# Kernel optimization log

Measured on AMD Instinct MI355X. Metric: run time of the kernel, lower is better.

The kernel has to match this reference:

```python
import jax, jax.numpy as jnp
import numpy as np

N = 50000
E = 1_600_000
IN_C = 128
HID = 64
HEADS = 2
OUT_C = 16
NEG_SLOPE = 0.2
EPS = 1e-16


def setup_inputs() -> dict:
    key = jax.random.key(0)
    ks = jax.random.split(key, 10)
    x = jax.random.normal(ks[0], (N, IN_C), dtype=jnp.float32)
    edge_index = jax.random.randint(ks[1], (2, E), 0, N, dtype=jnp.int64)
    # layer 1: in -> HEADS * HID, concat=True
    s1 = 1.0 / np.sqrt(IN_C)
    W1 = jax.random.normal(ks[2], (IN_C, HEADS * HID), dtype=jnp.float32) * s1
    att_src1 = jax.random.normal(ks[3], (HEADS, HID), dtype=jnp.float32) * (1.0 / np.sqrt(HID))
    att_dst1 = jax.random.normal(ks[4], (HEADS, HID), dtype=jnp.float32) * (1.0 / np.sqrt(HID))
    b1 = jnp.zeros((HEADS * HID,), dtype=jnp.float32)
    # layer 2: HEADS*HID -> OUT_C, heads=1
    s2 = 1.0 / np.sqrt(HEADS * HID)
    W2 = jax.random.normal(ks[5], (HEADS * HID, OUT_C), dtype=jnp.float32) * s2
    att_src2 = jax.random.normal(ks[6], (1, OUT_C), dtype=jnp.float32) * (1.0 / np.sqrt(OUT_C))
    att_dst2 = jax.random.normal(ks[7], (1, OUT_C), dtype=jnp.float32) * (1.0 / np.sqrt(OUT_C))
    b2 = jnp.zeros((OUT_C,), dtype=jnp.float32)
    return {"x": x, "W1": W1, "att_src1": att_src1, "att_dst1": att_dst1, "b1": b1,
            "W2": W2, "att_src2": att_src2, "att_dst2": att_dst2, "b2": b2,
            "edge_index": edge_index}


def gat_conv(x, edge_index, W, att_src, att_dst, bias, heads, out_ch):
    """PyG-style GATConv: per-head linear, additive attention, softmax over
    incoming edges of each destination node, scatter-add aggregation."""
    n = x.shape[0]
    src, dst = edge_index[0], edge_index[1]
    h = (x @ W).reshape(n, heads, out_ch)                # [N,H,C]
    a_src = jnp.einsum('nhc,hc->nh', h, att_src)          # [N,H]
    a_dst = jnp.einsum('nhc,hc->nh', h, att_dst)          # [N,H]
    e = a_src[src] + a_dst[dst]                           # [E,H]
    e = jnp.where(e >= 0, e, NEG_SLOPE * e)               # LeakyReLU(0.2)
    e_max = jax.ops.segment_max(e, dst, num_segments=n)   # [N,H]
    e_max = jax.lax.stop_gradient(jnp.where(jnp.isfinite(e_max), e_max, 0.0))
    e_exp = jnp.exp(e - e_max[dst])                       # [E,H]
    denom = jax.ops.segment_sum(e_exp, dst, num_segments=n)  # [N,H]
    alpha = e_exp / (denom[dst] + EPS)                    # [E,H]
    msg = h[src] * alpha[:, :, None]                      # [E,H,C] (dominant traffic)
    out = jax.ops.segment_sum(msg, dst, num_segments=n)   # [N,H,C]
    return out.reshape(n, heads * out_ch) + bias


def reference(x, W1, att_src1, att_dst1, b1, W2, att_src2, att_dst2, b2, edge_index):
    h = gat_conv(x, edge_index, W1, att_src1, att_dst1, b1, HEADS, HID)
    h = jax.nn.elu(h)
    h = gat_conv(h, edge_index, W2, att_src2, att_dst2, b2, 1, OUT_C)
    return jax.nn.softmax(h, axis=1)
```

## Files before the change

### kernel.cpp

```cpp
#include <hip/hip_runtime.h>
#include <hip/hip_fp16.h>
#include <cstdint>
#include <cstddef>

#define N_NODES 50000
#define N_EDGES 1600000
#define NEG_SLOPE 0.2f
#define GAT_EPS 1e-16f

#define NCHUNK 128
#define CE (N_EDGES / NCHUNK)
#define NBKT 196
#define GEMM_BLOCKS 782

typedef _Float16 half8v __attribute__((ext_vector_type(8)));
typedef _Float16 half4v __attribute__((ext_vector_type(4)));
typedef float f32x4 __attribute__((ext_vector_type(4)));



__global__ __launch_bounds__(256) void k_gh(
    const float* __restrict__ x, const float* __restrict__ W1,
    const float* __restrict__ W2, const float* __restrict__ b1,
    const float* __restrict__ att_src, const float* __restrict__ att_dst,
    _Float16* __restrict__ h1p, float* __restrict__ a_src, float* __restrict__ a_dst,
    const int* __restrict__ ei, int* __restrict__ coarse,
    float* __restrict__ w2tp, float* __restrict__ b1p) {
    __shared__ __align__(16) char smem[34816];
    int t = threadIdx.x;
    int b = blockIdx.x;
    if (b == GEMM_BLOCKS + NCHUNK) {
        for (int i = t; i < 2112; i += 256) {
            int j = i / 132, kp = i % 132;
            float v = 0.f;
            if (kp < 128) {
                int real = (kp & 7) * 16 + (kp >> 3);
                v = W2[real * 16 + j];
            }
            w2tp[i] = v;
        }
        if (t < 128) {
            int real = (t & 7) * 16 + (t >> 3);
            b1p[t] = b1[real];
        }
        return;
    }
    if (b >= GEMM_BLOCKS) {
        int* h = (int*)smem;
        int g = b - GEMM_BLOCKS;
        int wv = t >> 6;
        for (int i = t; i < 1024; i += 256) h[i] = 0;
        __syncthreads();
        int* hw = h + (wv << 8);
        int e0 = g * CE;
        for (int e = e0 + t; e < e0 + CE; e += 256)
            atomicAdd(&hw[ei[N_EDGES + e] >> 8], 1);
        __syncthreads();
        if (t < NBKT) coarse[t * NCHUNK + g] = h[t] + h[256 + t] + h[512 + t] + h[768 + t];
        return;
    }
    _Float16* wl = (_Float16*)smem;
    for (int j = t; j < 16384; j += 256) {
        int k = j >> 7, c = j & 127;
        wl[c * 136 + k] = (_Float16)W1[j];
    }
    __syncthreads();
    int wv = t >> 6, lane = t & 63;
    int m = lane & 15, q = lane >> 4;
    int nb = b * 64 + wv * 16;
    int grow = nb + m;
    const float* xrow = x + (size_t)((grow < N_NODES) ? grow : (N_NODES - 1)) * 128;
    f32x4 acc[8];
#pragma unroll
    for (int ct = 0; ct < 8; ++ct) acc[ct] = (f32x4){0.f, 0.f, 0.f, 0.f};
#pragma unroll
    for (int kc = 0; kc < 4; ++kc) {
        float4 u0 = *(const float4*)(xrow + kc * 32 + q * 8);
        float4 u1 = *(const float4*)(xrow + kc * 32 + q * 8 + 4);
        half8v a;
        a[0] = (_Float16)u0.x; a[1] = (_Float16)u0.y;
        a[2] = (_Float16)u0.z; a[3] = (_Float16)u0.w;
        a[4] = (_Float16)u1.x; a[5] = (_Float16)u1.y;
        a[6] = (_Float16)u1.z; a[7] = (_Float16)u1.w;
#pragma unroll
        for (int ct = 0; ct < 8; ++ct) {
            half8v bf = *(const half8v*)(wl + (ct * 16 + m) * 136 + kc * 32 + q * 8);
            acc[ct] = __builtin_amdgcn_mfma_f32_16x16x32_f16(a, bf, acc[ct], 0, 0, 0);
        }
    }
    float att_s[8], att_d[8];
#pragma unroll
    for (int ct = 0; ct < 8; ++ct) {
        att_s[ct] = att_src[ct * 16 + m];
        att_d[ct] = att_dst[ct * 16 + m];
    }
#pragma unroll
    for (int r = 0; r < 4; ++r) {
        int gn = nb + q * 4 + r;
        half8v hv;
        float ps0 = 0.f, ps1 = 0.f, pd0 = 0.f, pd1 = 0.f;
#pragma unroll
        for (int ct = 0; ct < 8; ++ct) {
            float v = acc[ct][r];
            hv[ct] = (_Float16)v;
            if (ct < 4) { ps0 += v * att_s[ct]; pd0 += v * att_d[ct]; }
            else        { ps1 += v * att_s[ct]; pd1 += v * att_d[ct]; }
        }
#pragma unroll
        for (int off = 8; off >= 1; off >>= 1) {
            ps0 += __shfl_xor(ps0, off, 64);
            ps1 += __shfl_xor(ps1, off, 64);
            pd0 += __shfl_xor(pd0, off, 64);
            pd1 += __shfl_xor(pd1, off, 64);
        }
        if (gn < N_NODES) {
            *(half8v*)(h1p + (size_t)gn * 128 + m * 8) = hv;
            if (m == 0) {
                a_src[gn * 2 + 0] = ps0;
                a_src[gn * 2 + 1] = ps1;
                a_dst[gn * 2 + 0] = pd0;
                a_dst[gn * 2 + 1] = pd1;
            }
        }
    }
}


__global__ __launch_bounds__(1024) void k_cscan(const int* __restrict__ coarse,
                                                int* __restrict__ cbase,
                                                int* __restrict__ bb,
                                                int* __restrict__ row_start) {
    __shared__ int cl[NBKT * NCHUNK];
    __shared__ int btot[256];
    __shared__ int bbase[NBKT];
    __shared__ int wt4[4];
    int t = threadIdx.x;
    for (int i = t; i < NBKT * NCHUNK; i += 1024) cl[i] = coarse[i];
    __syncthreads();
    if (t < 256) {
        int s = 0;
        if (t < NBKT)
            for (int g = 0; g < NCHUNK; ++g) s += cl[t * NCHUNK + g];
        btot[t] = s;
        int lane = t & 63, w = t >> 6;
        int x = s;
#pragma unroll
        for (int off = 1; off < 64; off <<= 1) {
            int y = __shfl_up(x, off, 64);
            if (lane >= off) x += y;
        }
        if (lane == 63) wt4[w] = x;
        __syncthreads();
        int woff = 0;
        for (int i = 0; i < w; ++i) woff += wt4[i];
        if (t < NBKT) bbase[t] = woff + x - s;
    } else {
        __syncthreads();
    }
    __syncthreads();
    if (t < NBKT) {
        int run = bbase[t];
        bb[t] = run;
        for (int g = 0; g < NCHUNK; ++g) {
            cbase[t * NCHUNK + g] = run;
            run += cl[t * NCHUNK + g];
        }
    }
    if (t == 0) { bb[NBKT] = N_EDGES; row_start[N_NODES] = N_EDGES; }
}

__global__ __launch_bounds__(256) void k_partition(const int* __restrict__ ei,
                                                   const int* __restrict__ cbase,
                                                   unsigned int* __restrict__ part) {
    __shared__ int loc[NBKT];
    int t = threadIdx.x, g = blockIdx.x;
    if (t < NBKT) loc[t] = cbase[t * NCHUNK + g];
    __syncthreads();
    int e0 = g * CE;
    for (int e = e0 + t; e < e0 + CE; e += 256) {
        int s = ei[e], d = ei[N_EDGES + e];
        int slot = atomicAdd(&loc[d >> 8], 1);
        part[slot] = ((unsigned int)d << 16) | (unsigned int)s;
    }
}

__global__ __launch_bounds__(256) void k_local(const unsigned int* __restrict__ part,
                                               const int* __restrict__ bb,
                                               const float* __restrict__ a_src1,
                                               const float* __restrict__ a_dst1,
                                               int* __restrict__ row_start,
                                               int* __restrict__ csrc,
                                               float2* __restrict__ cw) {
    __shared__ int hist[256];
    __shared__ int fillv[256];
    __shared__ float2 adl[256];
    __shared__ int wtot[4];
    int t = threadIdx.x, b = blockIdx.x;
    int n0 = b << 8;
    int es = bb[b], ee = bb[b + 1];
    hist[t] = 0;
    if (n0 + t < N_NODES) adl[t] = ((const float2*)a_dst1)[n0 + t];
    __syncthreads();
    for (int e = es + t; e < ee; e += 256) atomicAdd(&hist[(part[e] >> 16) - n0], 1);
    __syncthreads();
    int lane = t & 63, w = t >> 6;
    int v = hist[t], x = v;
#pragma unroll
    for (int off = 1; off < 64; off <<= 1) {
        int y = __shfl_up(x, off, 64);
        if (lane >= off) x += y;
    }
    if (lane == 63) wtot[w] = x;
    __syncthreads();
    int woff = 0;
    for (int i = 0; i < w; ++i) woff += wtot[i];
    int excl = woff + x - v;
    if (n0 + t < N_NODES) row_start[n0 + t] = es + excl;
    fillv[t] = excl;
    __syncthreads();
    for (int e = es + t; e < ee; e += 256) {
        unsigned int sd = part[e];
        int s = (int)(sd & 0xFFFFu);
        int j = (int)(sd >> 16) - n0;
        int slot = es + atomicAdd(&fillv[j], 1);
        float2 as = ((const float2*)a_src1)[s];
        float2 ad = adl[j];
        float e0 = as.x + ad.x; e0 = (e0 >= 0.f) ? e0 : NEG_SLOPE * e0;
        float e1 = as.y + ad.y; e1 = (e1 >= 0.f) ? e1 : NEG_SLOPE * e1;
        csrc[slot] = s;
        cw[slot] = make_float2(expf(e0), expf(e1));
    }
}


__global__ __launch_bounds__(256) void k_agg1f(
    const int* __restrict__ row_start, const int* __restrict__ csrc,
    const float2* __restrict__ cw,
    const _Float16* __restrict__ h1p, const float* __restrict__ b1p,
    const float* __restrict__ w2tp,
    const float* __restrict__ att_src2, const float* __restrict__ att_dst2,
    float* __restrict__ h2, float* __restrict__ as2, float* __restrict__ ad2) {
    __shared__ float w2l[16 * 132];
    __shared__ float rows[4][128];
    __shared__ int4 elds[4][64];
    int t = threadIdx.x;
    for (int i = t; i < 528; i += 256) ((float4*)w2l)[i] = ((const float4*)w2tp)[i];
    __syncthreads();
    int wv = t >> 6, lane = t & 63;
    int d = blockIdx.x * 4 + wv;
    int row = row_start[d], end = row_start[d + 1];
    int m16 = lane & 15;
    int qt = lane >> 4;
    uint32_t moff = (uint32_t)m16 * 16u;
    const char* hbase = (const char*)h1p;
    float den0 = 0.f, den1 = 0.f;
    float acc[8];
#pragma unroll
    for (int i = 0; i < 8; ++i) acc[i] = 0.f;
    for (int base = row; base < end; base += 64) {
        int m = end - base;
        if (m > 64) m = 64;
        int idx = base + lane;
        int idxc = (idx < end) ? idx : (end - 1);
        int s = csrc[idxc];
        float2 wv2 = cw[idxc];
        if (idx >= end) { wv2.x = 0.f; wv2.y = 0.f; }
        elds[wv][lane] = make_int4(s, __float_as_int(wv2.x), __float_as_int(wv2.y), 0);
        int nc = (m + 3) >> 2;
        auto step = [&](int p) {
            int4 md = elds[wv][p * 4 + qt];
            float w0 = __int_as_float(md.y);
            float w1 = __int_as_float(md.z);
            uint32_t off = ((uint32_t)md.x << 8) + moff;
            half8v hv = *(const half8v*)(hbase + off);
            den0 += w0;
            den1 += w1;
            acc[0] += w0 * (float)hv[0];
            acc[1] += w0 * (float)hv[1];
            acc[2] += w0 * (float)hv[2];
            acc[3] += w0 * (float)hv[3];
            acc[4] += w1 * (float)hv[4];
            acc[5] += w1 * (float)hv[5];
            acc[6] += w1 * (float)hv[6];
            acc[7] += w1 * (float)hv[7];
        };
        int p = 0;
        for (; p + 4 <= nc; p += 4) {
            step(p); step(p + 1); step(p + 2); step(p + 3);
        }
        for (; p < nc; ++p) step(p);
    }
#pragma unroll
    for (int i = 0; i < 8; ++i) {
        acc[i] += __shfl_xor(acc[i], 16, 64);
        acc[i] += __shfl_xor(acc[i], 32, 64);
    }
    den0 += __shfl_xor(den0, 16, 64);
    den0 += __shfl_xor(den0, 32, 64);
    den1 += __shfl_xor(den1, 16, 64);
    den1 += __shfl_xor(den1, 32, 64);
    float inv0 = 1.f / (den0 + GAT_EPS);
    float inv1 = 1.f / (den1 + GAT_EPS);
    {
        int cbase2 = qt * 2;
        float inv = (cbase2 < 4) ? inv0 : inv1;
        float2 bv = *(const float2*)(b1p + m16 * 8 + cbase2);
        float oa = acc[cbase2] * inv + bv.x;
        float ob = acc[cbase2 + 1] * inv + bv.y;
        oa = (oa > 0.f) ? oa : expm1f(oa);
        ob = (ob > 0.f) ? ob : expm1f(ob);
        *(float2*)(&rows[wv][m16 * 8 + cbase2]) = make_float2(oa, ob);
    }
    int j = lane & 15, q = lane >> 4;
    const float* r = rows[wv];
    const float* wt = &w2l[j * 132];
    int k0 = q * 32;
    float acc2 = 0.f;
#pragma unroll
    for (int sI = 0; sI < 8; ++sI) {
        int sp = ((sI + q) & 7) * 4;
        float4 rv = *(const float4*)(r + k0 + sp);
        float4 w4 = *(const float4*)(wt + k0 + sp);
        acc2 += rv.x * w4.x + rv.y * w4.y + rv.z * w4.z + rv.w * w4.w;
    }
    acc2 += __shfl_xor(acc2, 16, 64);
    acc2 += __shfl_xor(acc2, 32, 64);
    if (lane < 16) {
        h2[(size_t)d * 16 + j] = acc2;
        float ps = acc2 * att_src2[j];
        float pd = acc2 * att_dst2[j];
#pragma unroll
        for (int off = 8; off >= 1; off >>= 1) {
            ps += __shfl_xor(ps, off, 64);
            pd += __shfl_xor(pd, off, 64);
        }
        if (lane == 0) { as2[d] = ps; ad2[d] = pd; }
    }
}


__global__ __launch_bounds__(256) void k_agg2(
    const int* __restrict__ row_start, const int* __restrict__ csrc,
    const float* __restrict__ h2, const float* __restrict__ as2,
    const float* __restrict__ ad2, const float* __restrict__ b2,
    float* __restrict__ out) {
    __shared__ int2 elds[4][64];
    int t = threadIdx.x;
    int wv = t >> 6, lane = t & 63;
    int d = blockIdx.x * 4 + wv;
    int row = row_start[d], end = row_start[d + 1];
    float ad = ad2[d];
    int g16 = lane >> 2;
    int cq = lane & 3;
    float den = 0.f;
    float ax = 0.f, ay = 0.f, az = 0.f, aw = 0.f;
    for (int base = row; base < end; base += 64) {
        int m = end - base;
        if (m > 64) m = 64;
        int idx = base + lane;
        int idxc = (idx < end) ? idx : (end - 1);
        int s = csrc[idxc];
        float w = 0.f;
        if (idx < end) {
            float e = as2[s] + ad;
            e = (e >= 0.f) ? e : NEG_SLOPE * e;
            w = expf(e);
        }
        den += w;
        elds[wv][lane] = make_int2(s, __float_as_int(w));
        int nc = (m + 15) >> 4;
        auto step = [&](int p) {
            int2 md = elds[wv][p * 16 + g16];
            float wj = __int_as_float(md.y);
            float4 hv = *(const float4*)(h2 + (size_t)md.x * 16 + cq * 4);
            ax += wj * hv.x;
            ay += wj * hv.y;
            az += wj * hv.z;
            aw += wj * hv.w;
        };
        int p = 0;
        for (; p + 4 <= nc; p += 4) {
            step(p); step(p + 1); step(p + 2); step(p + 3);
        }
        for (; p < nc; ++p) step(p);
    }
#pragma unroll
    for (int off = 32; off >= 1; off >>= 1) den += __shfl_xor(den, off, 64);
#pragma unroll
    for (int off = 4; off <= 32; off <<= 1) {
        ax += __shfl_xor(ax, off, 64);
        ay += __shfl_xor(ay, off, 64);
        az += __shfl_xor(az, off, 64);
        aw += __shfl_xor(aw, off, 64);
    }
    float inv = 1.f / (den + GAT_EPS);
    const float4 b4 = *(const float4*)(b2 + cq * 4);
    float v0 = ax * inv + b4.x;
    float v1 = ay * inv + b4.y;
    float v2 = az * inv + b4.z;
    float v3 = aw * inv + b4.w;
    float mmax = fmaxf(fmaxf(v0, v1), fmaxf(v2, v3));
    mmax = fmaxf(mmax, __shfl_xor(mmax, 1, 64));
    mmax = fmaxf(mmax, __shfl_xor(mmax, 2, 64));
    float e0 = expf(v0 - mmax);
    float e1 = expf(v1 - mmax);
    float e2 = expf(v2 - mmax);
    float e3 = expf(v3 - mmax);
    float sum = e0 + e1 + e2 + e3;
    sum += __shfl_xor(sum, 1, 64);
    sum += __shfl_xor(sum, 2, 64);
    float isum = 1.f / sum;
    if (g16 == 0)
        *(float4*)(out + (size_t)d * 16 + cq * 4) =
            make_float4(e0 * isum, e1 * isum, e2 * isum, e3 * isum);
}


extern "C" void kernel_launch(void* const* d_in, const int* in_sizes, int n_in,
                              void* d_out, int out_size, void* d_ws, size_t ws_size,
                              hipStream_t stream) {
    const float* x        = (const float*)d_in[0];
    const float* W1       = (const float*)d_in[1];
    const float* att_src1 = (const float*)d_in[2];
    const float* att_dst1 = (const float*)d_in[3];
    const float* b1       = (const float*)d_in[4];
    const float* W2       = (const float*)d_in[5];
    const float* att_src2 = (const float*)d_in[6];
    const float* att_dst2 = (const float*)d_in[7];
    const float* b2       = (const float*)d_in[8];
    const int*   ei       = (const int*)d_in[9];

    char* p = (char*)d_ws;
    auto alloc = [&](size_t bytes) {
        char* r = p;
        p += (bytes + 255) & ~(size_t)255;
        return r;
    };
    _Float16* h1p  = (_Float16*)alloc(sizeof(_Float16) * (size_t)N_NODES * 128);
    float* w2tp    = (float*)alloc(sizeof(float) * 16 * 132);
    float* b1p     = (float*)alloc(sizeof(float) * 128);
    float* h2      = (float*)alloc(sizeof(float) * (size_t)N_NODES * 16);
    float* a_src   = (float*)alloc(sizeof(float) * N_NODES * 2);
    float* a_dst   = (float*)alloc(sizeof(float) * N_NODES * 2);
    float* as2     = (float*)alloc(sizeof(float) * N_NODES);
    float* ad2     = (float*)alloc(sizeof(float) * N_NODES);
    int* coarse    = (int*)alloc(sizeof(int) * NBKT * NCHUNK);
    int* cbase     = (int*)alloc(sizeof(int) * NBKT * NCHUNK);
    int* bb        = (int*)alloc(sizeof(int) * (NBKT + 1));
    int* row_start = (int*)alloc(sizeof(int) * (N_NODES + 1));
    unsigned int* part = (unsigned int*)alloc(sizeof(unsigned int) * (size_t)N_EDGES);
    int* csrc      = (int*)alloc(sizeof(int) * (size_t)N_EDGES);
    float2* cw     = (float2*)alloc(sizeof(float2) * (size_t)N_EDGES);

    k_gh<<<GEMM_BLOCKS + NCHUNK + 1, 256, 0, stream>>>(x, W1, W2, b1, att_src1, att_dst1,
                                                       h1p, a_src, a_dst, ei, coarse, w2tp, b1p);
    k_cscan<<<1, 1024, 0, stream>>>(coarse, cbase, bb, row_start);
    k_partition<<<NCHUNK, 256, 0, stream>>>(ei, cbase, part);
    k_local<<<NBKT, 256, 0, stream>>>(part, bb, a_src, a_dst, row_start, csrc, cw);
    k_agg1f<<<N_NODES / 4, 256, 0, stream>>>(row_start, csrc, cw, h1p, b1p, w2tp, att_src2, att_dst2, h2, as2, ad2);
    k_agg2<<<N_NODES / 4, 256, 0, stream>>>(row_start, csrc, h2, as2, ad2, b2, (float*)d_out);
}
```

Baseline: 253.4 us.

## Transpose coarse histogram layout, vectorize W1 staging, batch gathers, nontemporal edge loads

The coarse bucket-count array is switched to chunk-major layout, so histogram writes and partition reads become coalesced. W1 is staged into shared memory with float4 loads instead of scalar loads. In the layer-1 aggregation kernel, eight neighbor-feature gathers are issued before any accumulation to raise memory-level parallelism, at the cost of more registers. CSR source and weight streams are read with nontemporal loads to avoid polluting cache.

```diff
diff --git a/kernel.cpp b/kernel.cpp
--- a/kernel.cpp
+++ b/kernel.cpp
@@ -56,13 +56,18 @@
         for (int e = e0 + t; e < e0 + CE; e += 256)
             atomicAdd(&hw[ei[N_EDGES + e] >> 8], 1);
         __syncthreads();
-        if (t < NBKT) coarse[t * NCHUNK + g] = h[t] + h[256 + t] + h[512 + t] + h[768 + t];
+        if (t < NBKT) coarse[g * NBKT + t] = h[t] + h[256 + t] + h[512 + t] + h[768 + t];
         return;
     }
     _Float16* wl = (_Float16*)smem;
-    for (int j = t; j < 16384; j += 256) {
-        int k = j >> 7, c = j & 127;
-        wl[c * 136 + k] = (_Float16)W1[j];
+    for (int j = t; j < 4096; j += 256) {
+        float4 v = ((const float4*)W1)[j];
+        int base = j * 4;
+        int k = base >> 7, c = base & 127;
+        wl[(c + 0) * 136 + k] = (_Float16)v.x;
+        wl[(c + 1) * 136 + k] = (_Float16)v.y;
+        wl[(c + 2) * 136 + k] = (_Float16)v.z;
+        wl[(c + 3) * 136 + k] = (_Float16)v.w;
     }
     __syncthreads();
     int wv = t >> 6, lane = t & 63;
@@ -140,7 +145,7 @@
     if (t < 256) {
         int s = 0;
         if (t < NBKT)
-            for (int g = 0; g < NCHUNK; ++g) s += cl[t * NCHUNK + g];
+            for (int g = 0; g < NCHUNK; ++g) s += cl[g * NBKT + t];
         btot[t] = s;
         int lane = t & 63, w = t >> 6;
         int x = s;
@@ -162,8 +167,8 @@
         int run = bbase[t];
         bb[t] = run;
         for (int g = 0; g < NCHUNK; ++g) {
-            cbase[t * NCHUNK + g] = run;
-            run += cl[t * NCHUNK + g];
+            cbase[g * NBKT + t] = run;
+            run += cl[g * NBKT + t];
         }
     }
     if (t == 0) { bb[NBKT] = N_EDGES; row_start[N_NODES] = N_EDGES; }
@@ -174,7 +179,7 @@
                                                    unsigned int* __restrict__ part) {
     __shared__ int loc[NBKT];
     int t = threadIdx.x, g = blockIdx.x;
-    if (t < NBKT) loc[t] = cbase[t * NCHUNK + g];
+    if (t < NBKT) loc[t] = cbase[g * NBKT + t];
     __syncthreads();
     int e0 = g * CE;
     for (int e = e0 + t; e < e0 + CE; e += 256) {
@@ -262,17 +267,17 @@
         if (m > 64) m = 64;
         int idx = base + lane;
         int idxc = (idx < end) ? idx : (end - 1);
-        int s = csrc[idxc];
-        float2 wv2 = cw[idxc];
+        int s = __builtin_nontemporal_load(&csrc[idxc]);
+        uint64_t wbits = __builtin_nontemporal_load((const uint64_t*)&cw[idxc]);
+        float2 wv2;
+        wv2.x = __int_as_float((uint32_t)wbits);
+        wv2.y = __int_as_float((uint32_t)(wbits >> 32));
         if (idx >= end) { wv2.x = 0.f; wv2.y = 0.f; }
         elds[wv][lane] = make_int4(s, __float_as_int(wv2.x), __float_as_int(wv2.y), 0);
         int nc = (m + 3) >> 2;
-        auto step = [&](int p) {
-            int4 md = elds[wv][p * 4 + qt];
+        auto acc_one = [&](const int4& md, const half8v& hv) {
             float w0 = __int_as_float(md.y);
             float w1 = __int_as_float(md.z);
-            uint32_t off = ((uint32_t)md.x << 8) + moff;
-            half8v hv = *(const half8v*)(hbase + off);
             den0 += w0;
             den1 += w1;
             acc[0] += w0 * (float)hv[0];
@@ -285,10 +290,22 @@
             acc[7] += w1 * (float)hv[7];
         };
         int p = 0;
-        for (; p + 4 <= nc; p += 4) {
-            step(p); step(p + 1); step(p + 2); step(p + 3);
-        }
-        for (; p < nc; ++p) step(p);
+        for (; p + 8 <= nc; p += 8) {
+            int4 md[8];
+#pragma unroll
+            for (int u = 0; u < 8; ++u) md[u] = elds[wv][(p + u) * 4 + qt];
+            half8v hv[8];
+#pragma unroll
+            for (int u = 0; u < 8; ++u)
+                hv[u] = *(const half8v*)(hbase + (((uint32_t)md[u].x) << 8) + moff);
+#pragma unroll
+            for (int u = 0; u < 8; ++u) acc_one(md[u], hv[u]);
+        }
+        for (; p < nc; ++p) {
+            int4 md = elds[wv][p * 4 + qt];
+            half8v hv = *(const half8v*)(hbase + (((uint32_t)md.x) << 8) + moff);
+            acc_one(md, hv);
+        }
     }
 #pragma unroll
     for (int i = 0; i < 8; ++i) {
@@ -359,7 +376,7 @@
         if (m > 64) m = 64;
         int idx = base + lane;
         int idxc = (idx < end) ? idx : (end - 1);
-        int s = csrc[idxc];
+        int s = __builtin_nontemporal_load(&csrc[idxc]);
         float w = 0.f;
         if (idx < end) {
             float e = as2[s] + ad;
```

Result: slower. 282.3 us (+11.4%).
